# Kernel tuning notes

Hardware: AMD Instinct MI355X
Metric: run time of the kernel (lower is better)

The kernel has to match this reference:

```python
import math
import jax, jax.numpy as jnp
import numpy as np

HEADS = 16

def setup_inputs() -> dict:
    key = jax.random.key(0)
    k1, k2, k3, k4, k5 = jax.random.split(key, 5)
    B, T, W = 2, 2048, 1024
    x = jax.random.normal(k1, (B, T, W), dtype=jnp.float32)
    # Linear params stored as [in, out] for x @ W + b
    W_qkv = jax.random.normal(k2, (W, 3 * W), dtype=jnp.float32) / math.sqrt(W)
    b_qkv = jnp.zeros((3 * W,), dtype=jnp.float32)
    W_proj = jax.random.normal(k3, (W, W), dtype=jnp.float32) / math.sqrt(W)
    b_proj = jnp.zeros((W,), dtype=jnp.float32)
    return {"x": x, "W_qkv": W_qkv, "b_qkv": b_qkv, "W_proj": W_proj, "b_proj": b_proj}


def reference(x, W_qkv, b_qkv, W_proj, b_proj):
    B, T, width = x.shape
    heads = HEADS
    attn_ch = width // heads  # == (3*width) // heads // 3
    scale = 1.0 / math.sqrt(math.sqrt(attn_ch))

    qkv = x @ W_qkv + b_qkv                      # [B, T, 3W]
    qkv = qkv.reshape(B, T, heads, 3 * attn_ch)
    q, k, v = jnp.split(qkv, 3, axis=-1)          # each [B, T, H, C]

    # manual attention with float32 softmax over full score matrix
    weight = jnp.einsum('bthc,bshc->bhts', q * scale, k * scale)
    weight = jax.nn.softmax(weight.astype(jnp.float32), axis=-1).astype(qkv.dtype)
    out = jnp.einsum('bhts,bshc->bthc', weight, v)  # [B, T, H, C]

    # adaptive position-wise weight from Q-K mean interaction
    k_mean = k.mean(axis=1)                                   # [B, H, C]
    interaction = jnp.einsum('bthc,bhc->bth', q * scale, k_mean * scale)
    pos = interaction.sum(axis=-1)                            # [B, T]
    mn = pos.min(axis=1, keepdims=True)
    mx = pos.max(axis=1, keepdims=True)
    aw = (pos - mn) / (mx - mn + 1e-6)                        # [B, T]

    out = aw[:, :, None, None] * out
    out = out.reshape(B, T, width)
    return out @ W_proj + b_proj
```

## Files before the change

### kernel.cpp

```cpp
#include <hip/hip_runtime.h>
#include <hip/hip_bf16.h>


#define LOG2E 1.4426950408889634f

typedef float f32x4 __attribute__((ext_vector_type(4)));
typedef short bf16x8 __attribute__((ext_vector_type(8)));

__device__ __forceinline__ unsigned short f2bf(float f) {
  union { float f; unsigned int u; } v; v.f = f;
  unsigned int r = v.u + 0x7fffu + ((v.u >> 16) & 1u);
  return (unsigned short)(r >> 16);
}
__device__ __forceinline__ float bf2f(unsigned short h) {
  union { unsigned int u; float f; } v; v.u = ((unsigned int)h) << 16;
  return v.f;
}
__device__ __forceinline__ unsigned int pk_bf16(float a, float b) {
  union { __hip_bfloat162 h; unsigned int u; } v;
  v.h = __float22bfloat162_rn(make_float2(a, b));
  return v.u;
}

__global__ __launch_bounds__(256) void conv_split(
    const float* __restrict__ in, unsigned short* __restrict__ hi,
    unsigned short* __restrict__ lo) {
  size_t base = ((size_t)blockIdx.x * 256 + threadIdx.x) * 8;
  float4 v0 = *(const float4*)&in[base];
  float4 v1 = *(const float4*)&in[base + 4];
  float f[8] = {v0.x, v0.y, v0.z, v0.w, v1.x, v1.y, v1.z, v1.w};
  unsigned int hw[4], lw[4];
#pragma unroll
  for (int p = 0; p < 4; ++p) {
    float a = f[2 * p], b = f[2 * p + 1];
    unsigned short ha = f2bf(a), hb = f2bf(b);
    unsigned short la = f2bf(a - bf2f(ha)), lb = f2bf(b - bf2f(hb));
    hw[p] = (unsigned int)ha | ((unsigned int)hb << 16);
    lw[p] = (unsigned int)la | ((unsigned int)lb << 16);
  }
  uint4 H = {hw[0], hw[1], hw[2], hw[3]};
  uint4 L = {lw[0], lw[1], lw[2], lw[3]};
  *(uint4*)&hi[base] = H;
  *(uint4*)&lo[base] = L;
}

__global__ __launch_bounds__(256) void conv_split_T(
    const float* __restrict__ in, unsigned short* __restrict__ hi,
    unsigned short* __restrict__ lo, int K, int N) {
  __shared__ float t[32][33];
  const int n0 = blockIdx.x * 32, k0 = blockIdx.y * 32;
  const int r = threadIdx.x >> 3, c4 = (threadIdx.x & 7) * 4;
  float4 v = *(const float4*)&in[(size_t)(k0 + r) * N + n0 + c4];
  t[r][c4 + 0] = v.x; t[r][c4 + 1] = v.y; t[r][c4 + 2] = v.z; t[r][c4 + 3] = v.w;
  __syncthreads();
  unsigned int hw[2], lw[2];
#pragma unroll
  for (int p = 0; p < 2; ++p) {
    float a = t[c4 + 2 * p][r], b = t[c4 + 2 * p + 1][r];
    unsigned short ha = f2bf(a), hb = f2bf(b);
    unsigned short la = f2bf(a - bf2f(ha)), lb = f2bf(b - bf2f(hb));
    hw[p] = (unsigned int)ha | ((unsigned int)hb << 16);
    lw[p] = (unsigned int)la | ((unsigned int)lb << 16);
  }
  size_t o = (size_t)(n0 + r) * K + k0 + c4;
  *(uint2*)&hi[o] = make_uint2(hw[0], hw[1]);
  *(uint2*)&lo[o] = make_uint2(lw[0], lw[1]);
}

__global__ __launch_bounds__(256, 2) void gemm_mfma_split(
    const unsigned short* __restrict__ Ah, const unsigned short* __restrict__ Al,
    const unsigned short* __restrict__ Bh, const unsigned short* __restrict__ Bl,
    const float* __restrict__ bias, float* __restrict__ C,
    int M, int N, int K) {
  __shared__ __align__(16) unsigned short lds[2][16384];

  const int tid = threadIdx.x;
  const int w = tid >> 6, l = tid & 63;
  const int lc = l & 15, lr = l >> 4;
  const int wr = w >> 1, wc = w & 1;
  const int m0 = blockIdx.y * 128, n0 = blockIdx.x * 128;

  f32x4 acc[4][4];
#pragma unroll
  for (int mi = 0; mi < 4; ++mi)
#pragma unroll
    for (int ni = 0; ni < 4; ++ni) acc[mi][ni] = (f32x4){0.f, 0.f, 0.f, 0.f};

  const unsigned short* src = (w == 0) ? Ah : (w == 1) ? Al : (w == 2) ? Bh : Bl;
  const int rowbase = (w < 2) ? m0 : n0;
  const int lrow = l >> 2, lkk = (l & 3) * 8;

  const int NT = K / 32;
  int buf = 0;

#define STAGE(B_, KT_)                                                         \
  {                                                                            \
    unsigned short* dst = lds[B_] + w * 4096;                                  \
    _Pragma("unroll") for (int c = 0; c < 8; ++c) {                            \
      const unsigned short* g =                                                \
          src + (size_t)(rowbase + c * 16 + lrow) * K + (KT_) + lkk;           \
      __builtin_amdgcn_global_load_lds(                                        \
          (const __attribute__((address_space(1))) unsigned int*)g,            \
          (__attribute__((address_space(3))) unsigned int*)(dst + c * 512),    \
          16, 0, 0);                                                           \
    }                                                                          \
  }

  STAGE(0, 0);
  asm volatile("s_waitcnt vmcnt(0)");
  __syncthreads();

  for (int t = 0; t < NT; ++t) {
    if (t + 1 < NT) STAGE(buf ^ 1, (t + 1) * 32);

    const unsigned short* bp = lds[buf];
    bf16x8 ah[4], al[4], bh[4], bl[4];
#pragma unroll
    for (int mi = 0; mi < 4; ++mi) {
      int ro = (wr * 64 + mi * 16 + lc) * 32 + lr * 8;
      ah[mi] = *(const bf16x8*)&bp[ro];
      al[mi] = *(const bf16x8*)&bp[4096 + ro];
    }
#pragma unroll
    for (int ni = 0; ni < 4; ++ni) {
      int co = (wc * 64 + ni * 16 + lc) * 32 + lr * 8;
      bh[ni] = *(const bf16x8*)&bp[8192 + co];
      bl[ni] = *(const bf16x8*)&bp[12288 + co];
    }

    __builtin_amdgcn_s_setprio(1);
#pragma unroll
    for (int mi = 0; mi < 4; ++mi)
#pragma unroll
      for (int ni = 0; ni < 4; ++ni) {
        acc[mi][ni] = __builtin_amdgcn_mfma_f32_16x16x32_bf16(ah[mi], bh[ni], acc[mi][ni], 0, 0, 0);
        acc[mi][ni] = __builtin_amdgcn_mfma_f32_16x16x32_bf16(ah[mi], bl[ni], acc[mi][ni], 0, 0, 0);
        acc[mi][ni] = __builtin_amdgcn_mfma_f32_16x16x32_bf16(al[mi], bh[ni], acc[mi][ni], 0, 0, 0);
      }
    __builtin_amdgcn_s_setprio(0);

    __syncthreads();
    buf ^= 1;
  }
#undef STAGE

#pragma unroll
  for (int mi = 0; mi < 4; ++mi)
#pragma unroll
    for (int r = 0; r < 4; ++r) {
      int row = m0 + wr * 64 + mi * 16 + lr * 4 + r;
#pragma unroll
      for (int ni = 0; ni < 4; ++ni) {
        int col = n0 + wc * 64 + ni * 16 + lc;
        C[(size_t)row * N + col] = acc[mi][ni][r] + bias[col];
      }
    }
}

__global__ __launch_bounds__(256, 2) void gemm_qkv_fused(
    const unsigned short* __restrict__ Ah, const unsigned short* __restrict__ Al,
    const unsigned short* __restrict__ Bh, const unsigned short* __restrict__ Bl,
    const float* __restrict__ bias,
    unsigned short* __restrict__ Qh, unsigned short* __restrict__ Ql,
    unsigned short* __restrict__ Ktg, unsigned short* __restrict__ Vtg) {
  const int M = 4096, N = 3072, K = 1024;
  (void)M; (void)N;
  __shared__ __align__(16) unsigned short lds[2][16384];

  const int tid = threadIdx.x;
  const int w = tid >> 6, l = tid & 63;
  const int lc = l & 15, lr = l >> 4;
  const int wr = w >> 1, wc = w & 1;
  const int m0 = blockIdx.y * 128, n0 = blockIdx.x * 128;

  f32x4 acc[4][4];
#pragma unroll
  for (int mi = 0; mi < 4; ++mi)
#pragma unroll
    for (int ni = 0; ni < 4; ++ni) acc[mi][ni] = (f32x4){0.f, 0.f, 0.f, 0.f};

  const unsigned short* src = (w == 0) ? Ah : (w == 1) ? Al : (w == 2) ? Bh : Bl;
  const int rowbase = (w < 2) ? m0 : n0;
  const int lrow = l >> 2, lkk = (l & 3) * 8;

  const int NT = K / 32;
  int buf = 0;

#define STAGEQ(B_, KT_)                                                        \
  {                                                                            \
    unsigned short* dst = lds[B_] + w * 4096;                                  \
    _Pragma("unroll") for (int c = 0; c < 8; ++c) {                            \
      const unsigned short* g =                                                \
          src + (size_t)(rowbase + c * 16 + lrow) * K + (KT_) + lkk;           \
      __builtin_amdgcn_global_load_lds(                                        \
          (const __attribute__((address_space(1))) unsigned int*)g,            \
          (__attribute__((address_space(3))) unsigned int*)(dst + c * 512),    \
          16, 0, 0);                                                           \
    }                                                                          \
  }

  STAGEQ(0, 0);
  asm volatile("s_waitcnt vmcnt(0)");
  __syncthreads();

  for (int t = 0; t < NT; ++t) {
    if (t + 1 < NT) STAGEQ(buf ^ 1, (t + 1) * 32);

    const unsigned short* bp = lds[buf];
    bf16x8 ah[4], al[4], bh[4], bl[4];
#pragma unroll
    for (int mi = 0; mi < 4; ++mi) {
      int ro = (wr * 64 + mi * 16 + lc) * 32 + lr * 8;
      ah[mi] = *(const bf16x8*)&bp[ro];
      al[mi] = *(const bf16x8*)&bp[4096 + ro];
    }
#pragma unroll
    for (int ni = 0; ni < 4; ++ni) {
      int co = (wc * 64 + ni * 16 + lc) * 32 + lr * 8;
      bh[ni] = *(const bf16x8*)&bp[8192 + co];
      bl[ni] = *(const bf16x8*)&bp[12288 + co];
    }

    __builtin_amdgcn_s_setprio(1);
#pragma unroll
    for (int mi = 0; mi < 4; ++mi)
#pragma unroll
      for (int ni = 0; ni < 4; ++ni) {
        acc[mi][ni] = __builtin_amdgcn_mfma_f32_16x16x32_bf16(ah[mi], bh[ni], acc[mi][ni], 0, 0, 0);
        acc[mi][ni] = __builtin_amdgcn_mfma_f32_16x16x32_bf16(ah[mi], bl[ni], acc[mi][ni], 0, 0, 0);
        acc[mi][ni] = __builtin_amdgcn_mfma_f32_16x16x32_bf16(al[mi], bh[ni], acc[mi][ni], 0, 0, 0);
      }
    __builtin_amdgcn_s_setprio(0);

    __syncthreads();
    buf ^= 1;
  }
#undef STAGEQ

  const float QS = 0.125f * LOG2E;
#pragma unroll
  for (int ni = 0; ni < 4; ++ni) {
    int col = n0 + wc * 64 + ni * 16 + lc;
    int h = col / 192;
    int rr = col - h * 192;
    float bs = bias[col];
    if (rr < 64) {
      int c = rr;
#pragma unroll
      for (int mi = 0; mi < 4; ++mi)
#pragma unroll
        for (int r = 0; r < 4; ++r) {
          int row = m0 + wr * 64 + mi * 16 + lr * 4 + r;
          int bb = row >> 11, tl = row & 2047;
          float v = (acc[mi][ni][r] + bs) * QS;
          unsigned short hh = f2bf(v);
          size_t off = ((size_t)(bb * 16 + h) * 2048 + tl) * 64 + c;
          Qh[off] = hh;
          Ql[off] = f2bf(v - bf2f(hh));
        }
    } else if (rr < 128) {
      int c2 = (rr - 64) * 2;
#pragma unroll
      for (int mi = 0; mi < 4; ++mi)
#pragma unroll
        for (int r = 0; r < 4; ++r) {
          int row = m0 + wr * 64 + mi * 16 + lr * 4 + r;
          int bb = row >> 11, tl = row & 2047;
          int s = tl & 63;
          size_t base = (size_t)((bb * 16 + h) * 32 + (tl >> 6)) * 4096;
          Ktg[base + (((s * 128 + c2) ^ ((s & 7) << 4)) >> 1)] =
              f2bf(acc[mi][ni][r] + bs);
        }
    } else {
      int cb = (rr - 128) * 128, csw = ((rr - 128) & 7) << 4;
#pragma unroll
      for (int mi = 0; mi < 4; ++mi)
#pragma unroll
        for (int r = 0; r < 4; ++r) {
          int row = m0 + wr * 64 + mi * 16 + lr * 4 + r;
          int bb = row >> 11, tl = row & 2047;
          int s = tl & 63;
          size_t base = (size_t)((bb * 16 + h) * 32 + (tl >> 6)) * 4096;
          Vtg[base + (((cb + s * 2) ^ csw) >> 1)] = f2bf(acc[mi][ni][r] + bs);
        }
    }
  }
}

__global__ __launch_bounds__(256, 4) void attn_mfma(
    const unsigned short* __restrict__ Qh, const unsigned short* __restrict__ Ql,
    const unsigned short* __restrict__ Ktg, const unsigned short* __restrict__ Vtg,
    const float* __restrict__ aw,
    unsigned short* __restrict__ A2h, unsigned short* __restrict__ A2l) {
  const int qt = blockIdx.x, bh = blockIdx.y;
  const int b = bh >> 4, h = bh & 15;
  const int tid = threadIdx.x;
  const int w = tid >> 6, l = tid & 63;
  const int lc = l & 15, lr = l >> 4;

  __shared__ __align__(16) unsigned short ldsKV[2][8192];
  __shared__ __align__(16) unsigned short ldsP[4096];
  unsigned short* Pl = ldsP + w * 1024;
  uint2* Pl2 = (uint2*)Pl;

  const int q0 = qt * 64 + w * 16;
  bf16x8 qh0, qh1, ql0, ql1;
  {
    size_t base = ((size_t)bh * 2048 + q0 + lc) * 64 + lr * 8;
    qh0 = *(const bf16x8*)&Qh[base];
    qh1 = *(const bf16x8*)&Qh[base + 32];
    ql0 = *(const bf16x8*)&Ql[base];
    ql1 = *(const bf16x8*)&Ql[base + 32];
  }

  int kidx0[4], kidx1[4];
#pragma unroll
  for (int st = 0; st < 4; ++st) {
    int row = st * 16 + lc;
    int sw = (row & 7) << 4;
    kidx0[st] = ((row * 128 + lr * 16) ^ sw) >> 1;
    kidx1[st] = ((row * 128 + 64 + lr * 16) ^ sw) >> 1;
  }
  int pwd[4];
  {
    int sw = (lc & 7) << 4;
#pragma unroll
    for (int st = 0; st < 4; ++st)
      pwd[st] = ((lc * 128 + st * 32 + lr * 8) ^ sw) >> 3;
  }

  f32x4 o[4];
  float m = -1e30f, lsum = 0.f;
#pragma unroll
  for (int ct = 0; ct < 4; ++ct) o[ct] = (f32x4){0.f, 0.f, 0.f, 0.f};

  const unsigned short* gsrc =
      ((w < 2) ? Ktg : Vtg) + (size_t)bh * 32 * 4096 + (w & 1) * 2048 + l * 8;
  unsigned short* ldst0 = &ldsKV[0][(w >> 1) * 4096 + (w & 1) * 2048];
  unsigned short* ldst1 = &ldsKV[1][(w >> 1) * 4096 + (w & 1) * 2048];

#define STAGE_KV(DST_, T_)                                                     \
  {                                                                            \
    const unsigned short* g = gsrc + (size_t)(T_) * 4096;                      \
    _Pragma("unroll") for (int i = 0; i < 4; ++i) {                            \
      __builtin_amdgcn_global_load_lds(                                        \
          (const __attribute__((address_space(1))) unsigned int*)(g + i * 512),\
          (__attribute__((address_space(3))) unsigned int*)((DST_) + i * 512), \
          16, 0, 0);                                                           \
    }                                                                          \
  }

  STAGE_KV(ldst0, 0);
  asm volatile("s_waitcnt vmcnt(0)");
  __syncthreads();

  int buf = 0;
  for (int kvt = 0; kvt < 32; ++kvt) {
    if (kvt + 1 < 32) STAGE_KV(buf ? ldst0 : ldst1, kvt + 1);

    const unsigned short* KT = &ldsKV[buf][0];
    const unsigned short* VT = &ldsKV[buf][4096];

    f32x4 sacc[4];
    __builtin_amdgcn_s_setprio(1);
#pragma unroll
    for (int st = 0; st < 4; ++st) {
      bf16x8 k0 = *(const bf16x8*)&KT[kidx0[st]];
      bf16x8 k1 = *(const bf16x8*)&KT[kidx1[st]];
      f32x4 acc = (f32x4){0.f, 0.f, 0.f, 0.f};
      acc = __builtin_amdgcn_mfma_f32_16x16x32_bf16(k0, qh0, acc, 0, 0, 0);
      acc = __builtin_amdgcn_mfma_f32_16x16x32_bf16(k1, qh1, acc, 0, 0, 0);
      acc = __builtin_amdgcn_mfma_f32_16x16x32_bf16(k0, ql0, acc, 0, 0, 0);
      acc = __builtin_amdgcn_mfma_f32_16x16x32_bf16(k1, ql1, acc, 0, 0, 0);
      sacc[st] = acc;
    }
    __builtin_amdgcn_s_setprio(0);

    float pmax = fmaxf(fmaxf(fmaxf(sacc[0][0], sacc[0][1]), fmaxf(sacc[0][2], sacc[0][3])),
                       fmaxf(fmaxf(sacc[1][0], sacc[1][1]), fmaxf(sacc[1][2], sacc[1][3])));
    pmax = fmaxf(pmax,
           fmaxf(fmaxf(fmaxf(sacc[2][0], sacc[2][1]), fmaxf(sacc[2][2], sacc[2][3])),
                 fmaxf(fmaxf(sacc[3][0], sacc[3][1]), fmaxf(sacc[3][2], sacc[3][3]))));
    if (__any(pmax > m + 8.0f)) {
      float pm = fmaxf(pmax, __shfl_xor(pmax, 16));
      pm = fmaxf(pm, __shfl_xor(pm, 32));
      float mn = fmaxf(m, pm);
      float corr = exp2f(m - mn);
      m = mn;
      lsum *= corr;
#pragma unroll
      for (int r = 0; r < 4; ++r) {
        float cq = __shfl(corr, lr * 4 + r);
        o[0][r] *= cq; o[1][r] *= cq; o[2][r] *= cq; o[3][r] *= cq;
      }
    }

#pragma unroll
    for (int st = 0; st < 4; ++st)
#pragma unroll
      for (int r = 0; r < 4; ++r)
        sacc[st][r] = exp2f(sacc[st][r] - m);
#pragma unroll
    for (int st = 0; st < 4; ++st)
      lsum += (sacc[st][0] + sacc[st][1]) + (sacc[st][2] + sacc[st][3]);

#pragma unroll
    for (int st = 0; st < 4; ++st) {
      uint2 pv;
      pv.x = pk_bf16(sacc[st][0], sacc[st][1]);
      pv.y = pk_bf16(sacc[st][2], sacc[st][3]);
      Pl2[pwd[st]] = pv;
    }

    bf16x8 pa0 = *(const bf16x8*)&Pl[kidx0[0]];
    bf16x8 pa1 = *(const bf16x8*)&Pl[kidx1[0]];

    __builtin_amdgcn_s_setprio(1);
#pragma unroll
    for (int ct = 0; ct < 4; ++ct) {
      bf16x8 v0 = *(const bf16x8*)&VT[kidx0[ct]];
      bf16x8 v1 = *(const bf16x8*)&VT[kidx1[ct]];
      o[ct] = __builtin_amdgcn_mfma_f32_16x16x32_bf16(pa0, v0, o[ct], 0, 0, 0);
      o[ct] = __builtin_amdgcn_mfma_f32_16x16x32_bf16(pa1, v1, o[ct], 0, 0, 0);
    }
    __builtin_amdgcn_s_setprio(0);
    __syncthreads();
    buf ^= 1;
  }
#undef STAGE_KV

  lsum += __shfl_xor(lsum, 16);
  lsum += __shfl_xor(lsum, 32);
  float inv = 1.0f / lsum;
#pragma unroll
  for (int r = 0; r < 4; ++r) {
    int t = q0 + lr * 4 + r;
    float sc = aw[b * 2048 + t] * __shfl(inv, lr * 4 + r);
    size_t off = (size_t)(b * 2048 + t) * 1024 + h * 64 + lc;
#pragma unroll
    for (int ct = 0; ct < 4; ++ct) {
      float v = o[ct][r] * sc;
      unsigned short hh = f2bf(v);
      A2h[off + ct * 16] = hh;
      A2l[off + ct * 16] = f2bf(v - bf2f(hh));
    }
  }
}

__global__ __launch_bounds__(256) void kmean_part(
    const unsigned short* __restrict__ Ktg, float* __restrict__ kmp) {
  const int bh = blockIdx.x, seg = blockIdx.y;
  const int c = threadIdx.x & 63, sub = threadIdx.x >> 6;
  const int tile = seg * 4 + sub;
  const unsigned short* kt = Ktg + (size_t)(bh * 32 + tile) * 4096;
  float sum = 0.f;
#pragma unroll 8
  for (int s = 0; s < 64; ++s) {
    int sidx = ((s * 128 + c * 2) ^ ((s & 7) << 4)) >> 1;
    sum += bf2f(kt[sidx]);
  }
  __shared__ float red[4][64];
  red[sub][c] = sum;
  __syncthreads();
  if (sub == 0)
    kmp[(size_t)(bh * 8 + seg) * 64 + c] =
        red[0][c] + red[1][c] + red[2][c] + red[3][c];
}

__global__ __launch_bounds__(256) void pos_kernel(
    const unsigned short* __restrict__ Qh, const unsigned short* __restrict__ Ql,
    const float* __restrict__ kmp, float* __restrict__ pos) {
  __shared__ float kms[1024];
  int blk = blockIdx.x;
  int b = (blk * 4) >> 11;
  for (int i = threadIdx.x; i < 1024; i += 256) {
    int h = i >> 6, cc = i & 63;
    float s = 0.f;
#pragma unroll
    for (int seg = 0; seg < 8; ++seg)
      s += kmp[(size_t)((b * 16 + h) * 8 + seg) * 64 + cc];
    kms[i] = s * (1.0f / 2048.0f) * (1.0f / LOG2E);
  }
  __syncthreads();
  int w = threadIdx.x >> 6, lane = threadIdx.x & 63;
  int row = blk * 4 + w;
  int t = row & 2047;
  float p = 0.f;
#pragma unroll
  for (int h = 0; h < 16; ++h) {
    size_t idx = ((size_t)(b * 16 + h) * 2048 + t) * 64 + lane;
    p = fmaf(bf2f(Qh[idx]) + bf2f(Ql[idx]), kms[h * 64 + lane], p);
  }
#pragma unroll
  for (int off = 32; off; off >>= 1) p += __shfl_xor(p, off, 64);
  if (lane == 0) pos[row] = p;
}

__global__ __launch_bounds__(1024) void aw_kernel(const float* __restrict__ pos,
                                                  float* __restrict__ aw) {
  int b = blockIdx.x, tid = threadIdx.x;
  float p0 = pos[b * 2048 + tid], p1 = pos[b * 2048 + 1024 + tid];
  float mn = fminf(p0, p1), mx = fmaxf(p0, p1);
#pragma unroll
  for (int off = 32; off; off >>= 1) {
    mn = fminf(mn, __shfl_xor(mn, off, 64));
    mx = fmaxf(mx, __shfl_xor(mx, off, 64));
  }
  __shared__ float smn[16], smx[16];
  int wave = tid >> 6, lane = tid & 63;
  if (lane == 0) { smn[wave] = mn; smx[wave] = mx; }
  __syncthreads();
  if (tid < 64) {
    mn = (lane < 16) ? smn[lane] : 3.0e38f;
    mx = (lane < 16) ? smx[lane] : -3.0e38f;
#pragma unroll
    for (int off = 8; off; off >>= 1) {
      mn = fminf(mn, __shfl_xor(mn, off, 64));
      mx = fmaxf(mx, __shfl_xor(mx, off, 64));
    }
    if (lane == 0) { smn[0] = mn; smx[0] = mx; }
  }
  __syncthreads();
  float MN = smn[0], inv = 1.0f / (smx[0] - MN + 1e-6f);
  aw[b * 2048 + tid] = (p0 - MN) * inv;
  aw[b * 2048 + 1024 + tid] = (p1 - MN) * inv;
}

extern "C" void kernel_launch(void* const* d_in, const int* in_sizes, int n_in,
                              void* d_out, int out_size, void* d_ws, size_t ws_size,
                              hipStream_t stream) {
  const float* x      = (const float*)d_in[0];
  const float* W_qkv  = (const float*)d_in[1];
  const float* b_qkv  = (const float*)d_in[2];
  const float* W_proj = (const float*)d_in[3];
  const float* b_proj = (const float*)d_in[4];
  float* out = (float*)d_out;

  char* wsb = (char*)d_ws;
  unsigned short* xh  = (unsigned short*)wsb;
  unsigned short* xl  = xh + 4194304;
  unsigned short* A2h = (unsigned short*)wsb;
  unsigned short* A2l = A2h + 4194304;
  unsigned short* Wqh = (unsigned short*)(wsb + 16777216);
  unsigned short* Wql = Wqh + 3145728;
  unsigned short* Qh  = (unsigned short*)(wsb + 33554432);
  unsigned short* Ql  = Qh + 4194304;
  unsigned short* Ktg = Ql + 4194304;
  unsigned short* Vtg = Ktg + 4194304;
  unsigned short* Wph = (unsigned short*)(wsb + 67108864);
  unsigned short* Wpl = Wph + 1048576;
  float* kmp = (float*)(wsb + 71303168);
  float* pos = kmp + 16384;
  float* aw  = pos + 4096;

  conv_split<<<2048, 256, 0, stream>>>(x, xh, xl);
  conv_split_T<<<dim3(96, 32), 256, 0, stream>>>(W_qkv, Wqh, Wql, 1024, 3072);
  conv_split_T<<<dim3(32, 32), 256, 0, stream>>>(W_proj, Wph, Wpl, 1024, 1024);
  gemm_qkv_fused<<<dim3(24, 32), 256, 0, stream>>>(xh, xl, Wqh, Wql, b_qkv,
                                                   Qh, Ql, Ktg, Vtg);
  kmean_part<<<dim3(32, 8), 256, 0, stream>>>(Ktg, kmp);
  pos_kernel<<<1024, 256, 0, stream>>>(Qh, Ql, kmp, pos);
  aw_kernel<<<2, 1024, 0, stream>>>(pos, aw);
  attn_mfma<<<dim3(32, 32), 256, 0, stream>>>(Qh, Ql, Ktg, Vtg, aw, A2h, A2l);
  gemm_mfma_split<<<dim3(8, 32), 256, 0, stream>>>(A2h, A2l, Wph, Wpl, b_proj,
                                                   out, 4096, 1024, 1024);
}
```

Before: 294.7 us.

## Merge conversion kernels, use packed bf16 converts, unroll attention KV loop by two

```diff
diff --git a/kernel.cpp b/kernel.cpp
--- a/kernel.cpp
+++ b/kernel.cpp
@@ -17,39 +17,17 @@
   return v.f;
 }
 __device__ __forceinline__ unsigned int pk_bf16(float a, float b) {
-  union { __hip_bfloat162 h; unsigned int u; } v;
-  v.h = __float22bfloat162_rn(make_float2(a, b));
-  return v.u;
-}
-
-__global__ __launch_bounds__(256) void conv_split(
+  unsigned int r;
+  asm("v_cvt_pk_bf16_f32 %0, %1, %2" : "=v"(r) : "v"(a), "v"(b));
+  return r;
+}
+
+__device__ __forceinline__ void conv_T_tile(
     const float* __restrict__ in, unsigned short* __restrict__ hi,
-    unsigned short* __restrict__ lo) {
-  size_t base = ((size_t)blockIdx.x * 256 + threadIdx.x) * 8;
-  float4 v0 = *(const float4*)&in[base];
-  float4 v1 = *(const float4*)&in[base + 4];
-  float f[8] = {v0.x, v0.y, v0.z, v0.w, v1.x, v1.y, v1.z, v1.w};
-  unsigned int hw[4], lw[4];
-#pragma unroll
-  for (int p = 0; p < 4; ++p) {
-    float a = f[2 * p], b = f[2 * p + 1];
-    unsigned short ha = f2bf(a), hb = f2bf(b);
-    unsigned short la = f2bf(a - bf2f(ha)), lb = f2bf(b - bf2f(hb));
-    hw[p] = (unsigned int)ha | ((unsigned int)hb << 16);
-    lw[p] = (unsigned int)la | ((unsigned int)lb << 16);
-  }
-  uint4 H = {hw[0], hw[1], hw[2], hw[3]};
-  uint4 L = {lw[0], lw[1], lw[2], lw[3]};
-  *(uint4*)&hi[base] = H;
-  *(uint4*)&lo[base] = L;
-}
-
-__global__ __launch_bounds__(256) void conv_split_T(
-    const float* __restrict__ in, unsigned short* __restrict__ hi,
-    unsigned short* __restrict__ lo, int K, int N) {
-  __shared__ float t[32][33];
-  const int n0 = blockIdx.x * 32, k0 = blockIdx.y * 32;
-  const int r = threadIdx.x >> 3, c4 = (threadIdx.x & 7) * 4;
+    unsigned short* __restrict__ lo, int K, int N, int bx, int by,
+    float (*t)[33], int tid) {
+  const int n0 = bx * 32, k0 = by * 32;
+  const int r = tid >> 3, c4 = (tid & 7) * 4;
   float4 v = *(const float4*)&in[(size_t)(k0 + r) * N + n0 + c4];
   t[r][c4 + 0] = v.x; t[r][c4 + 1] = v.y; t[r][c4 + 2] = v.z; t[r][c4 + 3] = v.w;
   __syncthreads();
@@ -57,14 +35,50 @@
 #pragma unroll
   for (int p = 0; p < 2; ++p) {
     float a = t[c4 + 2 * p][r], b = t[c4 + 2 * p + 1][r];
-    unsigned short ha = f2bf(a), hb = f2bf(b);
-    unsigned short la = f2bf(a - bf2f(ha)), lb = f2bf(b - bf2f(hb));
-    hw[p] = (unsigned int)ha | ((unsigned int)hb << 16);
-    lw[p] = (unsigned int)la | ((unsigned int)lb << 16);
+    unsigned int h2 = pk_bf16(a, b);
+    float h0 = bf2f((unsigned short)h2), h1 = bf2f((unsigned short)(h2 >> 16));
+    hw[p] = h2;
+    lw[p] = pk_bf16(a - h0, b - h1);
   }
   size_t o = (size_t)(n0 + r) * K + k0 + c4;
   *(uint2*)&hi[o] = make_uint2(hw[0], hw[1]);
   *(uint2*)&lo[o] = make_uint2(lw[0], lw[1]);
+}
+
+__global__ __launch_bounds__(256) void conv_all(
+    const float* __restrict__ x, unsigned short* __restrict__ xh,
+    unsigned short* __restrict__ xl,
+    const float* __restrict__ Wq, unsigned short* __restrict__ Wqh,
+    unsigned short* __restrict__ Wql,
+    const float* __restrict__ Wp, unsigned short* __restrict__ Wph,
+    unsigned short* __restrict__ Wpl) {
+  __shared__ float t[32][33];
+  const int i = blockIdx.x, tid = threadIdx.x;
+  if (i < 2048) {
+    size_t base = ((size_t)i * 256 + tid) * 8;
+    float4 v0 = *(const float4*)&x[base];
+    float4 v1 = *(const float4*)&x[base + 4];
+    float f[8] = {v0.x, v0.y, v0.z, v0.w, v1.x, v1.y, v1.z, v1.w};
+    unsigned int hw[4], lw[4];
+#pragma unroll
+    for (int p = 0; p < 4; ++p) {
+      float a = f[2 * p], b = f[2 * p + 1];
+      unsigned int h2 = pk_bf16(a, b);
+      float h0 = bf2f((unsigned short)h2), h1 = bf2f((unsigned short)(h2 >> 16));
+      hw[p] = h2;
+      lw[p] = pk_bf16(a - h0, b - h1);
+    }
+    uint4 H = {hw[0], hw[1], hw[2], hw[3]};
+    uint4 L = {lw[0], lw[1], lw[2], lw[3]};
+    *(uint4*)&xh[base] = H;
+    *(uint4*)&xl[base] = L;
+  } else if (i < 5120) {
+    int j = i - 2048;
+    conv_T_tile(Wq, Wqh, Wql, 1024, 3072, j % 96, j / 96, t, tid);
+  } else {
+    int j = i - 5120;
+    conv_T_tile(Wp, Wph, Wpl, 1024, 1024, j % 32, j / 32, t, tid);
+  }
 }
 
 __global__ __launch_bounds__(256, 2) void gemm_mfma_split(
@@ -163,8 +177,7 @@
     const float* __restrict__ bias,
     unsigned short* __restrict__ Qh, unsigned short* __restrict__ Ql,
     unsigned short* __restrict__ Ktg, unsigned short* __restrict__ Vtg) {
-  const int M = 4096, N = 3072, K = 1024;
-  (void)M; (void)N;
+  const int K = 1024;
   __shared__ __align__(16) unsigned short lds[2][16384];
 
   const int tid = threadIdx.x;
@@ -249,39 +262,50 @@
 #pragma unroll
       for (int mi = 0; mi < 4; ++mi)
 #pragma unroll
-        for (int r = 0; r < 4; ++r) {
-          int row = m0 + wr * 64 + mi * 16 + lr * 4 + r;
+        for (int rp = 0; rp < 2; ++rp) {
+          int row = m0 + wr * 64 + mi * 16 + lr * 4 + rp * 2;
           int bb = row >> 11, tl = row & 2047;
-          float v = (acc[mi][ni][r] + bs) * QS;
-          unsigned short hh = f2bf(v);
+          float v0 = (acc[mi][ni][rp * 2] + bs) * QS;
+          float v1 = (acc[mi][ni][rp * 2 + 1] + bs) * QS;
+          unsigned int hw = pk_bf16(v0, v1);
+          float h0 = bf2f((unsigned short)hw), h1 = bf2f((unsigned short)(hw >> 16));
+          unsigned int lw = pk_bf16(v0 - h0, v1 - h1);
           size_t off = ((size_t)(bb * 16 + h) * 2048 + tl) * 64 + c;
-          Qh[off] = hh;
-          Ql[off] = f2bf(v - bf2f(hh));
+          Qh[off] = (unsigned short)hw;
+          Qh[off + 64] = (unsigned short)(hw >> 16);
+          Ql[off] = (unsigned short)lw;
+          Ql[off + 64] = (unsigned short)(lw >> 16);
         }
     } else if (rr < 128) {
       int c2 = (rr - 64) * 2;
 #pragma unroll
       for (int mi = 0; mi < 4; ++mi)
 #pragma unroll
-        for (int r = 0; r < 4; ++r) {
-          int row = m0 + wr * 64 + mi * 16 + lr * 4 + r;
+        for (int rp = 0; rp < 2; ++rp) {
+          int row = m0 + wr * 64 + mi * 16 + lr * 4 + rp * 2;
           int bb = row >> 11, tl = row & 2047;
           int s = tl & 63;
           size_t base = (size_t)((bb * 16 + h) * 32 + (tl >> 6)) * 4096;
+          unsigned int hw = pk_bf16(acc[mi][ni][rp * 2] + bs,
+                                    acc[mi][ni][rp * 2 + 1] + bs);
           Ktg[base + (((s * 128 + c2) ^ ((s & 7) << 4)) >> 1)] =
-              f2bf(acc[mi][ni][r] + bs);
+              (unsigned short)hw;
+          Ktg[base + ((((s + 1) * 128 + c2) ^ (((s + 1) & 7) << 4)) >> 1)] =
+              (unsigned short)(hw >> 16);
         }
     } else {
       int cb = (rr - 128) * 128, csw = ((rr - 128) & 7) << 4;
 #pragma unroll
       for (int mi = 0; mi < 4; ++mi)
 #pragma unroll
-        for (int r = 0; r < 4; ++r) {
-          int row = m0 + wr * 64 + mi * 16 + lr * 4 + r;
+        for (int rp = 0; rp < 2; ++rp) {
+          int row = m0 + wr * 64 + mi * 16 + lr * 4 + rp * 2;
           int bb = row >> 11, tl = row & 2047;
           int s = tl & 63;
           size_t base = (size_t)((bb * 16 + h) * 32 + (tl >> 6)) * 4096;
-          Vtg[base + (((cb + s * 2) ^ csw) >> 1)] = f2bf(acc[mi][ni][r] + bs);
+          unsigned int pv = pk_bf16(acc[mi][ni][rp * 2] + bs,
+                                    acc[mi][ni][rp * 2 + 1] + bs);
+          *(unsigned int*)&Vtg[base + (((cb + s * 2) ^ csw) >> 1)] = pv;
         }
     }
   }
@@ -354,78 +378,80 @@
   asm volatile("s_waitcnt vmcnt(0)");
   __syncthreads();
 
-  int buf = 0;
-  for (int kvt = 0; kvt < 32; ++kvt) {
-    if (kvt + 1 < 32) STAGE_KV(buf ? ldst0 : ldst1, kvt + 1);
-
-    const unsigned short* KT = &ldsKV[buf][0];
-    const unsigned short* VT = &ldsKV[buf][4096];
-
-    f32x4 sacc[4];
-    __builtin_amdgcn_s_setprio(1);
-#pragma unroll
-    for (int st = 0; st < 4; ++st) {
-      bf16x8 k0 = *(const bf16x8*)&KT[kidx0[st]];
-      bf16x8 k1 = *(const bf16x8*)&KT[kidx1[st]];
-      f32x4 acc = (f32x4){0.f, 0.f, 0.f, 0.f};
-      acc = __builtin_amdgcn_mfma_f32_16x16x32_bf16(k0, qh0, acc, 0, 0, 0);
-      acc = __builtin_amdgcn_mfma_f32_16x16x32_bf16(k1, qh1, acc, 0, 0, 0);
-      acc = __builtin_amdgcn_mfma_f32_16x16x32_bf16(k0, ql0, acc, 0, 0, 0);
-      acc = __builtin_amdgcn_mfma_f32_16x16x32_bf16(k1, ql1, acc, 0, 0, 0);
-      sacc[st] = acc;
-    }
-    __builtin_amdgcn_s_setprio(0);
-
-    float pmax = fmaxf(fmaxf(fmaxf(sacc[0][0], sacc[0][1]), fmaxf(sacc[0][2], sacc[0][3])),
-                       fmaxf(fmaxf(sacc[1][0], sacc[1][1]), fmaxf(sacc[1][2], sacc[1][3])));
-    pmax = fmaxf(pmax,
-           fmaxf(fmaxf(fmaxf(sacc[2][0], sacc[2][1]), fmaxf(sacc[2][2], sacc[2][3])),
-                 fmaxf(fmaxf(sacc[3][0], sacc[3][1]), fmaxf(sacc[3][2], sacc[3][3]))));
-    if (__any(pmax > m + 8.0f)) {
-      float pm = fmaxf(pmax, __shfl_xor(pmax, 16));
-      pm = fmaxf(pm, __shfl_xor(pm, 32));
-      float mn = fmaxf(m, pm);
-      float corr = exp2f(m - mn);
-      m = mn;
-      lsum *= corr;
-#pragma unroll
-      for (int r = 0; r < 4; ++r) {
-        float cq = __shfl(corr, lr * 4 + r);
-        o[0][r] *= cq; o[1][r] *= cq; o[2][r] *= cq; o[3][r] *= cq;
-      }
-    }
-
-#pragma unroll
-    for (int st = 0; st < 4; ++st)
-#pragma unroll
-      for (int r = 0; r < 4; ++r)
-        sacc[st][r] = exp2f(sacc[st][r] - m);
-#pragma unroll
-    for (int st = 0; st < 4; ++st)
-      lsum += (sacc[st][0] + sacc[st][1]) + (sacc[st][2] + sacc[st][3]);
-
-#pragma unroll
-    for (int st = 0; st < 4; ++st) {
-      uint2 pv;
-      pv.x = pk_bf16(sacc[st][0], sacc[st][1]);
-      pv.y = pk_bf16(sacc[st][2], sacc[st][3]);
-      Pl2[pwd[st]] = pv;
-    }
-
-    bf16x8 pa0 = *(const bf16x8*)&Pl[kidx0[0]];
-    bf16x8 pa1 = *(const bf16x8*)&Pl[kidx1[0]];
-
-    __builtin_amdgcn_s_setprio(1);
-#pragma unroll
-    for (int ct = 0; ct < 4; ++ct) {
-      bf16x8 v0 = *(const bf16x8*)&VT[kidx0[ct]];
-      bf16x8 v1 = *(const bf16x8*)&VT[kidx1[ct]];
-      o[ct] = __builtin_amdgcn_mfma_f32_16x16x32_bf16(pa0, v0, o[ct], 0, 0, 0);
-      o[ct] = __builtin_amdgcn_mfma_f32_16x16x32_bf16(pa1, v1, o[ct], 0, 0, 0);
-    }
-    __builtin_amdgcn_s_setprio(0);
-    __syncthreads();
-    buf ^= 1;
+  for (int kvt = 0; kvt < 32; kvt += 2) {
+#pragma unroll
+    for (int hf = 0; hf < 2; ++hf) {
+      const int t2 = kvt + hf;
+      if (t2 + 1 < 32) STAGE_KV(hf ? ldst0 : ldst1, t2 + 1);
+
+      const unsigned short* KT = &ldsKV[hf][0];
+      const unsigned short* VT = &ldsKV[hf][4096];
+
+      f32x4 sacc[4];
+      __builtin_amdgcn_s_setprio(1);
+#pragma unroll
+      for (int st = 0; st < 4; ++st) {
+        bf16x8 k0 = *(const bf16x8*)&KT[kidx0[st]];
+        bf16x8 k1 = *(const bf16x8*)&KT[kidx1[st]];
+        f32x4 acc = (f32x4){0.f, 0.f, 0.f, 0.f};
+        acc = __builtin_amdgcn_mfma_f32_16x16x32_bf16(k0, qh0, acc, 0, 0, 0);
+        acc = __builtin_amdgcn_mfma_f32_16x16x32_bf16(k1, qh1, acc, 0, 0, 0);
+        acc = __builtin_amdgcn_mfma_f32_16x16x32_bf16(k0, ql0, acc, 0, 0, 0);
+        acc = __builtin_amdgcn_mfma_f32_16x16x32_bf16(k1, ql1, acc, 0, 0, 0);
+        sacc[st] = acc;
+      }
+      __builtin_amdgcn_s_setprio(0);
+
+      float pmax = fmaxf(fmaxf(fmaxf(sacc[0][0], sacc[0][1]), fmaxf(sacc[0][2], sacc[0][3])),
+                         fmaxf(fmaxf(sacc[1][0], sacc[1][1]), fmaxf(sacc[1][2], sacc[1][3])));
+      pmax = fmaxf(pmax,
+             fmaxf(fmaxf(fmaxf(sacc[2][0], sacc[2][1]), fmaxf(sacc[2][2], sacc[2][3])),
+                   fmaxf(fmaxf(sacc[3][0], sacc[3][1]), fmaxf(sacc[3][2], sacc[3][3]))));
+      if (__any(pmax > m + 8.0f)) {
+        float pm = fmaxf(pmax, __shfl_xor(pmax, 16));
+        pm = fmaxf(pm, __shfl_xor(pm, 32));
+        float mn = fmaxf(m, pm);
+        float corr = exp2f(m - mn);
+        m = mn;
+        lsum *= corr;
+#pragma unroll
+        for (int r = 0; r < 4; ++r) {
+          float cq = __shfl(corr, lr * 4 + r);
+          o[0][r] *= cq; o[1][r] *= cq; o[2][r] *= cq; o[3][r] *= cq;
+        }
+      }
+
+#pragma unroll
+      for (int st = 0; st < 4; ++st)
+#pragma unroll
+        for (int r = 0; r < 4; ++r)
+          sacc[st][r] = exp2f(sacc[st][r] - m);
+#pragma unroll
+      for (int st = 0; st < 4; ++st)
+        lsum += (sacc[st][0] + sacc[st][1]) + (sacc[st][2] + sacc[st][3]);
+
+#pragma unroll
+      for (int st = 0; st < 4; ++st) {
+        uint2 pv;
+        pv.x = pk_bf16(sacc[st][0], sacc[st][1]);
+        pv.y = pk_bf16(sacc[st][2], sacc[st][3]);
+        Pl2[pwd[st]] = pv;
+      }
+
+      bf16x8 pa0 = *(const bf16x8*)&Pl[kidx0[0]];
+      bf16x8 pa1 = *(const bf16x8*)&Pl[kidx1[0]];
+
+      __builtin_amdgcn_s_setprio(1);
+#pragma unroll
+      for (int ct = 0; ct < 4; ++ct) {
+        bf16x8 v0 = *(const bf16x8*)&VT[kidx0[ct]];
+        bf16x8 v1 = *(const bf16x8*)&VT[kidx1[ct]];
+        o[ct] = __builtin_amdgcn_mfma_f32_16x16x32_bf16(pa0, v0, o[ct], 0, 0, 0);
+        o[ct] = __builtin_amdgcn_mfma_f32_16x16x32_bf16(pa1, v1, o[ct], 0, 0, 0);
+      }
+      __builtin_amdgcn_s_setprio(0);
+      __syncthreads();
+    }
   }
 #undef STAGE_KV
 
@@ -553,9 +579,8 @@
   float* pos = kmp + 16384;
   float* aw  = pos + 4096;
 
-  conv_split<<<2048, 256, 0, stream>>>(x, xh, xl);
-  conv_split_T<<<dim3(96, 32), 256, 0, stream>>>(W_qkv, Wqh, Wql, 1024, 3072);
-  conv_split_T<<<dim3(32, 32), 256, 0, stream>>>(W_proj, Wph, Wpl, 1024, 1024);
+  conv_all<<<6144, 256, 0, stream>>>(x, xh, xl, W_qkv, Wqh, Wql,
+                                     W_proj, Wph, Wpl);
   gemm_qkv_fused<<<dim3(24, 32), 256, 0, stream>>>(xh, xl, Wqh, Wql, b_qkv,
                                                    Qh, Ql, Ktg, Vtg);
   kmean_part<<<dim3(32, 8), 256, 0, stream>>>(Ktg, kmp);
```

New measurement: 278.6 us. -5.4%, faster.
